# Optimization experiments

Measured on AMD Instinct MI355X. Metric: run time of the kernel, lower is better.

The kernel has to match this reference:

```python
import jax, jax.numpy as jnp
import numpy as np

T, NS, NH, NO = 8192, 512, 1024, 512


def setup_inputs() -> dict:
    key = jax.random.key(0)
    ks = jax.random.split(key, 12)
    f32 = jnp.float32
    x = jax.random.normal(ks[0], (T, NS), f32)
    s = 0.02
    inp = {
        "x": x,
        "w_ih0": jax.random.normal(ks[1], (4 * NH, NS), f32) * s,
        "w_hh0": jax.random.normal(ks[2], (4 * NH, NH), f32) * s,
        "b_ih0": jnp.zeros((4 * NH,), f32),
        "b_hh0": jnp.zeros((4 * NH,), f32),
        "w_ih1": jax.random.normal(ks[3], (4 * NH, NH), f32) * s,
        "w_hh1": jax.random.normal(ks[4], (4 * NH, NH), f32) * s,
        "b_ih1": jnp.zeros((4 * NH,), f32),
        "b_hh1": jnp.zeros((4 * NH,), f32),
        "w_pol": jax.random.normal(ks[5], (NO, NH), f32) * 0.01,
        "b_pol": jax.random.normal(ks[6], (NO,), f32) * 0.01,
        "w_val": jax.random.normal(ks[7], (1, NH), f32) * 0.01,
        "b_val": jax.random.normal(ks[8], (1,), f32) * 0.01,
    }
    return inp


def _lstm_cell(xt, h, c, w_ih, w_hh, b):
    # torch gate order: i, f, g, o
    z = w_ih @ xt + w_hh @ h + b  # [4H]
    i, f, g, o = jnp.split(z, 4)
    i, f, o = jax.nn.sigmoid(i), jax.nn.sigmoid(f), jax.nn.sigmoid(o)
    g = jnp.tanh(g)
    c_new = f * c + i * g
    h_new = o * jnp.tanh(c_new)
    return h_new, c_new


def reference(x, w_ih0, w_hh0, b_ih0, b_hh0, w_ih1, w_hh1, b_ih1, b_hh1,
              w_pol, b_pol, w_val, b_val):
    b0 = b_ih0 + b_hh0
    b1 = b_ih1 + b_hh1
    z = jnp.zeros((NH,), x.dtype)

    def step(carry, xt):
        h0, c0, h1, c1 = carry
        h0, c0 = _lstm_cell(xt, h0, c0, w_ih0, w_hh0, b0)
        h1, c1 = _lstm_cell(h0, h1, c1, w_ih1, w_hh1, b1)
        return (h0, c0, h1, c1), h1

    _, hs = jax.lax.scan(step, (z, z, z, z), x)  # hs: [T, NH]
    policy = jax.nn.softmax(hs @ w_pol.T + b_pol, axis=-1)[:, None, :]  # [T,1,NO]
    values = (hs @ w_val.T + b_val)[:, None, :]  # [T,1,1]
    return policy, values
```

## Files before the change

kernel.cpp:

```cpp
#include <hip/hip_runtime.h>
#include <stdint.h>
#include <stddef.h>

typedef _Float16 f16;
typedef _Float16 half2_t __attribute__((ext_vector_type(2)));
typedef _Float16 half8_t __attribute__((ext_vector_type(8)));
typedef float   float4_t __attribute__((ext_vector_type(4)));
typedef float   float2_t __attribute__((ext_vector_type(2)));

#define T_STEPS 8192
#define L0_BLOCKS 128

#define OFF_ZX   ((size_t)0)
#define OFF_HS   ((size_t)67108864)
#define OFF_R0   (OFF_HS + (size_t)16777216)
#define OFF_R1   (OFF_R0 + (size_t)262144)

__device__ __forceinline__ uint32_t packh(float a, float b) {
  half2_t h; h.x = (_Float16)a; h.y = (_Float16)b;
  return __builtin_bit_cast(uint32_t, h);
}

__device__ __forceinline__ float fdot2w(uint32_t w, uint32_t h, float c) {
#if __has_builtin(__builtin_amdgcn_fdot2)
  return __builtin_amdgcn_fdot2(__builtin_bit_cast(half2_t, w),
                                __builtin_bit_cast(half2_t, h), c, false);
#else
  half2_t a = __builtin_bit_cast(half2_t, w);
  half2_t b = __builtin_bit_cast(half2_t, h);
  return c + (float)a.x * (float)b.x + (float)a.y * (float)b.y;
#endif
}

__device__ __forceinline__ uint64_t ald64(const uint64_t* p) {
  return __hip_atomic_load(p, __ATOMIC_RELAXED, __HIP_MEMORY_SCOPE_AGENT);
}
__device__ __forceinline__ void ast64(uint64_t* p, uint64_t v) {
  __hip_atomic_store(p, v, __ATOMIC_RELAXED, __HIP_MEMORY_SCOPE_AGENT);
}

__device__ __forceinline__ float sigf(float x) { return 1.f / (1.f + __expf(-x)); }
__device__ __forceinline__ float tanhf_(float x) { return 2.f * sigf(2.f * x) - 1.f; }

__global__ void k_init(uint64_t* __restrict__ R) {
  int i = blockIdx.x * blockDim.x + threadIdx.x;
  if (i < (16 + 8) * 4 * 512) R[i] = 0ull;
}

template <bool A16, bool OUT16>
__global__ __launch_bounds__(256) void k_gemm(const void* __restrict__ Ap,
                                              const float* __restrict__ B,
                                              const float* __restrict__ bias0,
                                              const float* __restrict__ bias1,
                                              void* __restrict__ Cp,
                                              int N, int K, int lda) {
  __shared__ __align__(16) f16 As[128 * 40];
  __shared__ __align__(16) f16 Bs[128 * 40];
  int bn = blockIdx.x * 128, bm = blockIdx.y * 128;
  int tid = threadIdx.x;
  int w = tid >> 6, l = tid & 63;
  int m0w = (w >> 1) * 64, n0w = (w & 1) * 64;
  int lr = l & 15, q = l >> 4;
  int srow = tid >> 1, skoff = (tid & 1) * 16;

  float4_t acc[4][4];
#pragma unroll
  for (int i = 0; i < 4; ++i)
#pragma unroll
    for (int j = 0; j < 4; ++j) acc[i][j] = (float4_t){0.f, 0.f, 0.f, 0.f};

  for (int kt = 0; kt < K; kt += 32) {
    __syncthreads();
    if (A16) {
      const f16* Ah = (const f16*)Ap + (size_t)(bm + srow) * lda + kt + skoff;
      uint4 u0 = *(const uint4*)Ah;
      uint4 u1 = *(const uint4*)(Ah + 8);
      *(uint4*)&As[srow * 40 + skoff] = u0;
      *(uint4*)&As[srow * 40 + skoff + 8] = u1;
    } else {
      const float* Af = (const float*)Ap + (size_t)(bm + srow) * lda + kt + skoff;
      const float4_t* A4 = (const float4_t*)Af;
      float4_t f0 = A4[0], f1 = A4[1], f2 = A4[2], f3 = A4[3];
      half8_t h0 = {(f16)f0.x, (f16)f0.y, (f16)f0.z, (f16)f0.w,
                    (f16)f1.x, (f16)f1.y, (f16)f1.z, (f16)f1.w};
      half8_t h1 = {(f16)f2.x, (f16)f2.y, (f16)f2.z, (f16)f2.w,
                    (f16)f3.x, (f16)f3.y, (f16)f3.z, (f16)f3.w};
      *(half8_t*)&As[srow * 40 + skoff] = h0;
      *(half8_t*)&As[srow * 40 + skoff + 8] = h1;
    }
    {
      const float* Bf = B + (size_t)(bn + srow) * K + kt + skoff;
      const float4_t* B4 = (const float4_t*)Bf;
      float4_t f0 = B4[0], f1 = B4[1], f2 = B4[2], f3 = B4[3];
      half8_t h0 = {(f16)f0.x, (f16)f0.y, (f16)f0.z, (f16)f0.w,
                    (f16)f1.x, (f16)f1.y, (f16)f1.z, (f16)f1.w};
      half8_t h1 = {(f16)f2.x, (f16)f2.y, (f16)f2.z, (f16)f2.w,
                    (f16)f3.x, (f16)f3.y, (f16)f3.z, (f16)f3.w};
      *(half8_t*)&Bs[srow * 40 + skoff] = h0;
      *(half8_t*)&Bs[srow * 40 + skoff + 8] = h1;
    }
    __syncthreads();
    half8_t af[4], bf[4];
#pragma unroll
    for (int i = 0; i < 4; ++i) af[i] = *(const half8_t*)&As[(m0w + 16 * i + lr) * 40 + q * 8];
#pragma unroll
    for (int j = 0; j < 4; ++j) bf[j] = *(const half8_t*)&Bs[(n0w + 16 * j + lr) * 40 + q * 8];
#pragma unroll
    for (int i = 0; i < 4; ++i)
#pragma unroll
      for (int j = 0; j < 4; ++j)
        acc[i][j] = __builtin_amdgcn_mfma_f32_16x16x32_f16(af[i], bf[j], acc[i][j], 0, 0, 0);
  }

#pragma unroll
  for (int j = 0; j < 4; ++j) {
    int n = bn + n0w + 16 * j + lr;
    float bv = bias0 ? bias0[n] : 0.f;
    if (bias1) bv += bias1[n];
#pragma unroll
    for (int i = 0; i < 4; ++i) {
#pragma unroll
      for (int r = 0; r < 4; ++r) {
        int m = bm + m0w + 16 * i + q * 4 + r;
        float v = acc[i][j][r] + bv;
        if (OUT16) ((f16*)Cp)[(size_t)m * N + n] = (f16)v;
        else       ((float*)Cp)[(size_t)m * N + n] = v;
      }
    }
  }
}

__global__ __launch_bounds__(256, 1) void k_serial(
    const f16* __restrict__ Zx,
    const float* __restrict__ whh0, const float* __restrict__ wih1,
    const float* __restrict__ whh1,
    uint64_t* __restrict__ R0, uint64_t* __restrict__ R1, f16* __restrict__ hs,
    const float* __restrict__ b_ih1, const float* __restrict__ b_hh1) {
  __shared__ __align__(8) uint32_t hL[1024];
  __shared__ uint32_t pairs[4];

  int tid = threadIdx.x, w = tid >> 6, l = tid & 63;

  if (blockIdx.x < L0_BLOCKS) {
    int b = blockIdx.x;
    uint32_t wr[64];
#pragma unroll
    for (int g = 0; g < 4; ++g)
#pragma unroll
      for (int o = 0; o < 2; ++o) {
        size_t R = (size_t)(1024 * g + 8 * b + 2 * w + o) * 1024;
#pragma unroll
        for (int p = 0; p < 8; ++p) {
          int k = l + 64 * p;
          float2_t u = *(const float2_t*)&whh0[R + 2 * k];
          wr[(2 * g + o) * 8 + p] = packh(u.x, u.y);
        }
      }
    float c0 = 0.f;
    float zx[4] = {0.f, 0.f, 0.f, 0.f};
    if (l < 2) {
#pragma unroll
      for (int g = 0; g < 4; ++g)
        zx[g] = (float)Zx[(size_t)1024 * g + 8 * b + 2 * w + l];
    }

    for (int t = 0; t < T_STEPS; ++t) {
      float zxn[4] = {0.f, 0.f, 0.f, 0.f};
      if (l < 2 && t + 1 < T_STEPS) {
#pragma unroll
        for (int g = 0; g < 4; ++g)
          zxn[g] = (float)Zx[(size_t)(t + 1) * 4096 + 1024 * g + 8 * b + 2 * w + l];
      }
      if (tid == 0 && t >= 2) {
        const uint64_t* lp =
            R1 + ((size_t)(b & 7) * 4 + (size_t)((t - 1) & 3)) * 512 + ((4 * b) & 511);
        while ((int)(uint32_t)(ald64(lp) >> 32) < t - 1) {}
      }
      {
        const uint64_t* base = R0 + ((size_t)(b & 7) * 4 + (size_t)(t & 3)) * 512;
        uint64_t v0 = 0, v1 = 0;
        bool d0 = false, d1 = false;
        do {
          if (!d0) { v0 = ald64(base + tid);       d0 = ((uint32_t)(v0 >> 32) == (uint32_t)t); }
          if (!d1) { v1 = ald64(base + tid + 256); d1 = ((uint32_t)(v1 >> 32) == (uint32_t)t); }
        } while (!(d0 && d1));
        hL[tid] = (uint32_t)v0;
        hL[tid + 256] = (uint32_t)v1;
      }
      __syncthreads();

      uint32_t hw[8];
#pragma unroll
      for (int p = 0; p < 8; ++p) hw[p] = hL[l + 64 * p];
      float acc[8];
#pragma unroll
      for (int ri = 0; ri < 8; ++ri) acc[ri] = 0.f;
#pragma unroll
      for (int ri = 0; ri < 8; ++ri)
#pragma unroll
        for (int p = 0; p < 8; ++p) acc[ri] = fdot2w(wr[ri * 8 + p], hw[p], acc[ri]);
#pragma unroll
      for (int d = 1; d < 64; d <<= 1)
#pragma unroll
        for (int ri = 0; ri < 8; ++ri) acc[ri] += __shfl_xor(acc[ri], d);

      float h = 0.f;
      if (l < 2) {
        float zi = acc[0 + l] + zx[0];
        float zf = acc[2 + l] + zx[1];
        float zg = acc[4 + l] + zx[2];
        float zo = acc[6 + l] + zx[3];
        float ig = sigf(zi), fg = sigf(zf), gg = tanhf_(zg), og = sigf(zo);
        c0 = fg * c0 + ig * gg;
        h = og * tanhf_(c0);
      }
      float ho = __shfl(h, 1);
      if (l == 0) pairs[w] = packh(h, ho);
      __syncthreads();
      if (w == 0) {
        uint64_t val = ((uint64_t)(uint32_t)(t + 1) << 32) | (uint64_t)pairs[l & 3];
        ast64(&R0[((size_t)(l >> 2) * 4 + (size_t)((t + 1) & 3)) * 512 + 4 * b + (l & 3)], val);
      }
#pragma unroll
      for (int g = 0; g < 4; ++g) zx[g] = zxn[g];
    }
  } else {
    int b = blockIdx.x - L0_BLOCKS;
    uint32_t wI[64], wH[64];
#pragma unroll
    for (int g = 0; g < 4; ++g)
#pragma unroll
      for (int o = 0; o < 2; ++o) {
        size_t R = (size_t)(1024 * g + 8 * b + 2 * w + o) * 1024;
#pragma unroll
        for (int p = 0; p < 8; ++p) {
          int k = l + 64 * p;
          float2_t u1 = *(const float2_t*)&wih1[R + 2 * k];
          float2_t u2 = *(const float2_t*)&whh1[R + 2 * k];
          wI[(2 * g + o) * 8 + p] = packh(u1.x, u1.y);
          wH[(2 * g + o) * 8 + p] = packh(u2.x, u2.y);
        }
      }
    float c1 = 0.f;
    float b1v[4] = {0.f, 0.f, 0.f, 0.f};
    if (l < 2) {
#pragma unroll
      for (int g = 0; g < 4; ++g) {
        int r = 1024 * g + 8 * b + 2 * w + l;
        b1v[g] = b_ih1[r] + b_hh1[r];
      }
    }

    for (int t = 0; t < T_STEPS; ++t) {
      {
        const uint64_t* b1p = R1 + ((size_t)(b & 7) * 4 + (size_t)(t & 3)) * 512;
        const uint64_t* b0p = R0 + ((size_t)(8 + (b & 7)) * 4 + (size_t)((t + 1) & 3)) * 512;
        uint64_t v0 = 0, v1 = 0, v2 = 0, v3 = 0;
        bool d0 = false, d1 = false, d2 = false, d3 = false;
        uint32_t tg0 = (uint32_t)(t + 1), tg1 = (uint32_t)t;
        do {
          if (!d0) { v0 = ald64(b0p + tid);       d0 = ((uint32_t)(v0 >> 32) == tg0); }
          if (!d1) { v1 = ald64(b0p + tid + 256); d1 = ((uint32_t)(v1 >> 32) == tg0); }
          if (!d2) { v2 = ald64(b1p + tid);       d2 = ((uint32_t)(v2 >> 32) == tg1); }
          if (!d3) { v3 = ald64(b1p + tid + 256); d3 = ((uint32_t)(v3 >> 32) == tg1); }
        } while (!(d0 && d1 && d2 && d3));
        hL[tid] = (uint32_t)v0;
        hL[tid + 256] = (uint32_t)v1;
        hL[512 + tid] = (uint32_t)v2;
        hL[768 + tid] = (uint32_t)v3;
      }
      __syncthreads();

      uint32_t h0w[8], h1w[8];
#pragma unroll
      for (int p = 0; p < 8; ++p) {
        h0w[p] = hL[l + 64 * p];
        h1w[p] = hL[512 + l + 64 * p];
      }
      float acc[8];
#pragma unroll
      for (int ri = 0; ri < 8; ++ri) acc[ri] = 0.f;
#pragma unroll
      for (int ri = 0; ri < 8; ++ri)
#pragma unroll
        for (int p = 0; p < 8; ++p) {
          acc[ri] = fdot2w(wI[ri * 8 + p], h0w[p], acc[ri]);
          acc[ri] = fdot2w(wH[ri * 8 + p], h1w[p], acc[ri]);
        }
#pragma unroll
      for (int d = 1; d < 64; d <<= 1)
#pragma unroll
        for (int ri = 0; ri < 8; ++ri) acc[ri] += __shfl_xor(acc[ri], d);

      float h = 0.f;
      if (l < 2) {
        float zi = acc[0 + l] + b1v[0];
        float zf = acc[2 + l] + b1v[1];
        float zg = acc[4 + l] + b1v[2];
        float zo = acc[6 + l] + b1v[3];
        float ig = sigf(zi), fg = sigf(zf), gg = tanhf_(zg), og = sigf(zo);
        c1 = fg * c1 + ig * gg;
        h = og * tanhf_(c1);
      }
      float ho = __shfl(h, 1);
      if (l == 0) {
        uint32_t pr = packh(h, ho);
        pairs[w] = pr;
        *(uint32_t*)(hs + (size_t)t * 1024 + 8 * b + 2 * w) = pr;
      }
      __syncthreads();
      if (w == 0 && l < 32) {
        uint64_t val = ((uint64_t)(uint32_t)(t + 1) << 32) | (uint64_t)pairs[l & 3];
        ast64(&R1[((size_t)(l >> 2) * 4 + (size_t)((t + 1) & 3)) * 512 + 4 * b + (l & 3)], val);
      }
    }
  }
}

__global__ void k_values(const f16* __restrict__ hs, const float* __restrict__ w_val,
                         const float* __restrict__ b_val, float* __restrict__ outv) {
  int t = blockIdx.x * 4 + (threadIdx.x >> 6);
  int l = threadIdx.x & 63;
  const f16* row = hs + (size_t)t * 1024 + l * 16;
  const float* wv = w_val + l * 16;
  float s = 0.f;
#pragma unroll
  for (int i = 0; i < 16; ++i) s += (float)row[i] * wv[i];
#pragma unroll
  for (int d = 1; d < 64; d <<= 1) s += __shfl_xor(s, d);
  if (l == 0) outv[t] = s + b_val[0];
}

__global__ void k_softmax(float* __restrict__ out) {
  int t = blockIdx.x * 4 + (threadIdx.x >> 6);
  int l = threadIdx.x & 63;
  float* row = out + (size_t)t * 512;
  float v[8];
  float m = -1e30f;
#pragma unroll
  for (int i = 0; i < 8; ++i) { v[i] = row[l + 64 * i]; m = fmaxf(m, v[i]); }
#pragma unroll
  for (int d = 1; d < 64; d <<= 1) m = fmaxf(m, __shfl_xor(m, d));
  float s = 0.f;
#pragma unroll
  for (int i = 0; i < 8; ++i) { v[i] = __expf(v[i] - m); s += v[i]; }
#pragma unroll
  for (int d = 1; d < 64; d <<= 1) s += __shfl_xor(s, d);
  float inv = 1.f / s;
#pragma unroll
  for (int i = 0; i < 8; ++i) row[l + 64 * i] = v[i] * inv;
}

extern "C" void kernel_launch(void* const* d_in, const int* in_sizes, int n_in,
                              void* d_out, int out_size, void* d_ws, size_t ws_size,
                              hipStream_t stream) {
  const float* x      = (const float*)d_in[0];
  const float* w_ih0  = (const float*)d_in[1];
  const float* w_hh0  = (const float*)d_in[2];
  const float* b_ih0  = (const float*)d_in[3];
  const float* b_hh0  = (const float*)d_in[4];
  const float* w_ih1  = (const float*)d_in[5];
  const float* w_hh1  = (const float*)d_in[6];
  const float* b_ih1  = (const float*)d_in[7];
  const float* b_hh1  = (const float*)d_in[8];
  const float* w_pol  = (const float*)d_in[9];
  const float* b_pol  = (const float*)d_in[10];
  const float* w_val  = (const float*)d_in[11];
  const float* b_val  = (const float*)d_in[12];

  char* ws = (char*)d_ws;
  f16*      Zx  = (f16*)(ws + OFF_ZX);
  f16*      hs  = (f16*)(ws + OFF_HS);
  uint64_t* R0  = (uint64_t*)(ws + OFF_R0);
  uint64_t* R1  = (uint64_t*)(ws + OFF_R1);
  float*    out = (float*)d_out;

  k_init<<<192, 256, 0, stream>>>(R0);
  k_gemm<false, true><<<dim3(32, 64), 256, 0, stream>>>(
      (const void*)x, w_ih0, b_ih0, b_hh0, (void*)Zx, 4096, 512, 512);
  k_serial<<<256, 256, 0, stream>>>(Zx, w_hh0, w_ih1, w_hh1, R0, R1, hs, b_ih1, b_hh1);
  k_gemm<true, false><<<dim3(4, 64), 256, 0, stream>>>(
      (const void*)hs, w_pol, b_pol, nullptr, (void*)out, 512, 1024, 1024);
  k_values<<<2048, 256, 0, stream>>>(hs, w_val, b_val, out + (size_t)8192 * 512);
  k_softmax<<<2048, 256, 0, stream>>>(out);
}
```

Before: 23.47 ms.

## Partition persistent LSTM recurrence by XCD with pipelined layer-1 input projection

Reworks the persistent recurrent kernel into 1024-thread blocks. Each block reads its XCD id and is assigned a role: layer-0 recurrence, layer-1 recurrence, or layer-1 input-projection producers. Layer-0/layer-1 recurrences each run in 32 blocks confined to one XCD and exchange h through XCD-local ring buffers. Layer-1's W_ih·h0 is computed ahead by separate blocks and passed via a tagged ring with progress counters for back-pressure. The intent is to shorten the per-step critical path by keeping tight polling within one XCD's L2 (polling with sc0 loads) and moving work off the serial path. The cost is a complex dependence on the hardware XCD layout, on all blocks being co-resident, and on a role-assignment handshake.

Measured after the change: 34.75 ms. +48.1%, slower.

```diff
diff --git a/kernel.cpp b/kernel.cpp
--- a/kernel.cpp
+++ b/kernel.cpp
@@ -9,18 +9,26 @@
 typedef float   float2_t __attribute__((ext_vector_type(2)));
 
 #define T_STEPS 8192
-#define L0_BLOCKS 128
 
 #define OFF_ZX   ((size_t)0)
 #define OFF_HS   ((size_t)67108864)
-#define OFF_R0   (OFF_HS + (size_t)16777216)
-#define OFF_R1   (OFF_R0 + (size_t)262144)
+#define OFF_R0A  ((size_t)83886080)
+#define OFF_R0B  (OFF_R0A + 131072)
+#define OFF_R1A  (OFF_R0B + 524288)
+#define OFF_ZR   (OFF_R1A + 131072)
+#define OFF_PG0  (OFF_ZR + 1048576)
+#define OFF_PG1  (OFF_PG0 + 8192)
+#define OFF_XC   (OFF_PG1 + 4096)
+#define ZERO_BYTES ((size_t)(OFF_XC + 1024 - OFF_R0A))
 
 __device__ __forceinline__ uint32_t packh(float a, float b) {
   half2_t h; h.x = (_Float16)a; h.y = (_Float16)b;
   return __builtin_bit_cast(uint32_t, h);
 }
-
+__device__ __forceinline__ float hlf(uint32_t u, int i) {
+  half2_t h = __builtin_bit_cast(half2_t, u);
+  return i ? (float)h.y : (float)h.x;
+}
 __device__ __forceinline__ float fdot2w(uint32_t w, uint32_t h, float c) {
 #if __has_builtin(__builtin_amdgcn_fdot2)
   return __builtin_amdgcn_fdot2(__builtin_bit_cast(half2_t, w),
@@ -31,20 +39,60 @@
   return c + (float)a.x * (float)b.x + (float)a.y * (float)b.y;
 #endif
 }
-
 __device__ __forceinline__ uint64_t ald64(const uint64_t* p) {
   return __hip_atomic_load(p, __ATOMIC_RELAXED, __HIP_MEMORY_SCOPE_AGENT);
 }
 __device__ __forceinline__ void ast64(uint64_t* p, uint64_t v) {
   __hip_atomic_store(p, v, __ATOMIC_RELAXED, __HIP_MEMORY_SCOPE_AGENT);
 }
-
+__device__ __forceinline__ uint32_t ald32(const uint32_t* p) {
+  return __hip_atomic_load(p, __ATOMIC_RELAXED, __HIP_MEMORY_SCOPE_AGENT);
+}
+__device__ __forceinline__ void ast32(uint32_t* p, uint32_t v) {
+  __hip_atomic_store(p, v, __ATOMIC_RELAXED, __HIP_MEMORY_SCOPE_AGENT);
+}
+__device__ __forceinline__ uint64_t l2ld64(const uint64_t* p) {
+  uint64_t v;
+  asm volatile("global_load_dwordx2 %0, %1, off sc0\n\ts_waitcnt vmcnt(0)"
+               : "=v"(v) : "v"(p) : "memory");
+  return v;
+}
+__device__ __forceinline__ uint32_t xcc_id() {
+  uint32_t x;
+  asm("s_getreg_b32 %0, hwreg(20, 0, 4)" : "=s"(x));
+  return x;
+}
+__device__ __forceinline__ uint32_t poll_fast(const uint64_t* p, uint32_t tag) {
+  int it = 0;
+  for (;;) {
+    uint64_t v = l2ld64(p);
+    if ((uint32_t)(v >> 32) == tag) return (uint32_t)v;
+    if ((++it & 7) == 7) {
+      v = ald64(p);
+      if ((uint32_t)(v >> 32) == tag) return (uint32_t)v;
+    }
+  }
+}
+__device__ __forceinline__ uint32_t poll_slow(const uint64_t* p, uint32_t tag) {
+  int it = 0;
+  for (;;) {
+    uint64_t v = l2ld64(p);
+    if ((uint32_t)(v >> 32) == tag) return (uint32_t)v;
+    if ((++it & 7) == 7) {
+      v = ald64(p);
+      if ((uint32_t)(v >> 32) == tag) return (uint32_t)v;
+      __builtin_amdgcn_s_sleep(1);
+    }
+  }
+}
 __device__ __forceinline__ float sigf(float x) { return 1.f / (1.f + __expf(-x)); }
 __device__ __forceinline__ float tanhf_(float x) { return 2.f * sigf(2.f * x) - 1.f; }
 
-__global__ void k_init(uint64_t* __restrict__ R) {
-  int i = blockIdx.x * blockDim.x + threadIdx.x;
-  if (i < (16 + 8) * 4 * 512) R[i] = 0ull;
+__global__ void k_init(uint64_t* __restrict__ Z) {
+  size_t n = ZERO_BYTES / 8;
+  for (size_t i = blockIdx.x * blockDim.x + threadIdx.x; i < n;
+       i += (size_t)gridDim.x * blockDim.x)
+    Z[i] = 0ull;
 }
 
 template <bool A16, bool OUT16>
@@ -111,7 +159,6 @@
       for (int j = 0; j < 4; ++j)
         acc[i][j] = __builtin_amdgcn_mfma_f32_16x16x32_f16(af[i], bf[j], acc[i][j], 0, 0, 0);
   }
-
 #pragma unroll
   for (int j = 0; j < 4; ++j) {
     int n = bn + n0w + 16 * j + lr;
@@ -130,191 +177,258 @@
   }
 }
 
-__global__ __launch_bounds__(256, 1) void k_serial(
-    const f16* __restrict__ Zx,
-    const float* __restrict__ whh0, const float* __restrict__ wih1,
-    const float* __restrict__ whh1,
-    uint64_t* __restrict__ R0, uint64_t* __restrict__ R1, f16* __restrict__ hs,
-    const float* __restrict__ b_ih1, const float* __restrict__ b_hh1) {
-  __shared__ __align__(8) uint32_t hL[1024];
-  __shared__ uint32_t pairs[4];
-
+__device__ __forceinline__ void run_l0(int r, const f16* Zx, const float* whh0,
+                                       uint64_t* R0A, uint64_t* R0B,
+                                       const uint32_t* prog0) {
+  __shared__ uint32_t hL[512];
+  __shared__ float zL[4][32];
+  __shared__ uint32_t pairsL[16];
   int tid = threadIdx.x, w = tid >> 6, l = tid & 63;
-
-  if (blockIdx.x < L0_BLOCKS) {
-    int b = blockIdx.x;
-    uint32_t wr[64];
-#pragma unroll
-    for (int g = 0; g < 4; ++g)
-#pragma unroll
-      for (int o = 0; o < 2; ++o) {
-        size_t R = (size_t)(1024 * g + 8 * b + 2 * w + o) * 1024;
-#pragma unroll
-        for (int p = 0; p < 8; ++p) {
-          int k = l + 64 * p;
-          float2_t u = *(const float2_t*)&whh0[R + 2 * k];
-          wr[(2 * g + o) * 8 + p] = packh(u.x, u.y);
-        }
+  int g = w & 3, hh = w >> 2;
+  int O = 32 * r;
+  uint32_t wr[64];
+#pragma unroll
+  for (int j = 0; j < 8; ++j) {
+    size_t R = (size_t)(1024 * g + O + 8 * hh + j) * 1024;
+#pragma unroll
+    for (int p = 0; p < 8; ++p) {
+      int k = l + 64 * p;
+      float2_t u = *(const float2_t*)&whh0[R + 2 * k];
+      wr[j * 8 + p] = packh(u.x, u.y);
+    }
+  }
+  float c0 = 0.f;
+  bool gl = (w == 0 && l < 32);
+  float zx[4] = {0, 0, 0, 0};
+  if (gl)
+#pragma unroll
+    for (int gi = 0; gi < 4; ++gi) zx[gi] = (float)Zx[(size_t)1024 * gi + O + l];
+  uint32_t pw0 = 0, pw1 = 0;
+  const uint32_t* pp0 = prog0 + (2 * r) * 32;
+  const uint32_t* pp1 = prog0 + (2 * r + 1) * 32;
+
+  for (int t = 0; t < T_STEPS; ++t) {
+    float zn[4] = {0, 0, 0, 0};
+    if (gl && t + 1 < T_STEPS)
+#pragma unroll
+      for (int gi = 0; gi < 4; ++gi)
+        zn[gi] = (float)Zx[(size_t)(t + 1) * 4096 + 1024 * gi + O + l];
+    if (tid == 512) {
+      uint32_t pm = pw0 < pw1 ? pw0 : pw1;
+      while (pm + 12 < (uint32_t)t) {
+        pw0 = ald32(pp0); pw1 = ald32(pp1);
+        pm = pw0 < pw1 ? pw0 : pw1;
       }
-    float c0 = 0.f;
-    float zx[4] = {0.f, 0.f, 0.f, 0.f};
-    if (l < 2) {
-#pragma unroll
-      for (int g = 0; g < 4; ++g)
-        zx[g] = (float)Zx[(size_t)1024 * g + 8 * b + 2 * w + l];
-    }
-
-    for (int t = 0; t < T_STEPS; ++t) {
-      float zxn[4] = {0.f, 0.f, 0.f, 0.f};
-      if (l < 2 && t + 1 < T_STEPS) {
-#pragma unroll
-        for (int g = 0; g < 4; ++g)
-          zxn[g] = (float)Zx[(size_t)(t + 1) * 4096 + 1024 * g + 8 * b + 2 * w + l];
-      }
-      if (tid == 0 && t >= 2) {
-        const uint64_t* lp =
-            R1 + ((size_t)(b & 7) * 4 + (size_t)((t - 1) & 3)) * 512 + ((4 * b) & 511);
-        while ((int)(uint32_t)(ald64(lp) >> 32) < t - 1) {}
-      }
-      {
-        const uint64_t* base = R0 + ((size_t)(b & 7) * 4 + (size_t)(t & 3)) * 512;
-        uint64_t v0 = 0, v1 = 0;
-        bool d0 = false, d1 = false;
-        do {
-          if (!d0) { v0 = ald64(base + tid);       d0 = ((uint32_t)(v0 >> 32) == (uint32_t)t); }
-          if (!d1) { v1 = ald64(base + tid + 256); d1 = ((uint32_t)(v1 >> 32) == (uint32_t)t); }
-        } while (!(d0 && d1));
-        hL[tid] = (uint32_t)v0;
-        hL[tid + 256] = (uint32_t)v1;
-      }
-      __syncthreads();
-
-      uint32_t hw[8];
-#pragma unroll
-      for (int p = 0; p < 8; ++p) hw[p] = hL[l + 64 * p];
-      float acc[8];
-#pragma unroll
-      for (int ri = 0; ri < 8; ++ri) acc[ri] = 0.f;
-#pragma unroll
-      for (int ri = 0; ri < 8; ++ri)
-#pragma unroll
-        for (int p = 0; p < 8; ++p) acc[ri] = fdot2w(wr[ri * 8 + p], hw[p], acc[ri]);
-#pragma unroll
-      for (int d = 1; d < 64; d <<= 1)
-#pragma unroll
-        for (int ri = 0; ri < 8; ++ri) acc[ri] += __shfl_xor(acc[ri], d);
-
+    }
+    if (tid < 512)
+      hL[tid] = poll_fast(R0A + ((size_t)((r & 3) * 8 + (t & 7)) * 512 + tid),
+                          (uint32_t)t);
+    __syncthreads();
+    uint32_t hw[8];
+#pragma unroll
+    for (int p = 0; p < 8; ++p) hw[p] = hL[l + 64 * p];
+    float acc[8];
+#pragma unroll
+    for (int j = 0; j < 8; ++j) acc[j] = 0.f;
+#pragma unroll
+    for (int j = 0; j < 8; ++j)
+#pragma unroll
+      for (int p = 0; p < 8; ++p) acc[j] = fdot2w(wr[j * 8 + p], hw[p], acc[j]);
+#pragma unroll
+    for (int d = 1; d < 64; d <<= 1)
+#pragma unroll
+      for (int j = 0; j < 8; ++j) acc[j] += __shfl_xor(acc[j], d);
+    if (l < 8) zL[g][8 * hh + l] = acc[l];
+    __syncthreads();
+    uint32_t tg = (uint32_t)(t + 1);
+    if (w == 0) {
       float h = 0.f;
-      if (l < 2) {
-        float zi = acc[0 + l] + zx[0];
-        float zf = acc[2 + l] + zx[1];
-        float zg = acc[4 + l] + zx[2];
-        float zo = acc[6 + l] + zx[3];
-        float ig = sigf(zi), fg = sigf(zf), gg = tanhf_(zg), og = sigf(zo);
+      if (l < 32) {
+        float zi = zL[0][l] + zx[0], zf = zL[1][l] + zx[1];
+        float zg_ = zL[2][l] + zx[2], zo = zL[3][l] + zx[3];
+        float ig = sigf(zi), fg = sigf(zf), gg = tanhf_(zg_), og = sigf(zo);
         c0 = fg * c0 + ig * gg;
         h = og * tanhf_(c0);
       }
-      float ho = __shfl(h, 1);
-      if (l == 0) pairs[w] = packh(h, ho);
-      __syncthreads();
-      if (w == 0) {
-        uint64_t val = ((uint64_t)(uint32_t)(t + 1) << 32) | (uint64_t)pairs[l & 3];
-        ast64(&R0[((size_t)(l >> 2) * 4 + (size_t)((t + 1) & 3)) * 512 + 4 * b + (l & 3)], val);
-      }
-#pragma unroll
-      for (int g = 0; g < 4; ++g) zx[g] = zxn[g];
-    }
-  } else {
-    int b = blockIdx.x - L0_BLOCKS;
-    uint32_t wI[64], wH[64];
-#pragma unroll
-    for (int g = 0; g < 4; ++g)
-#pragma unroll
-      for (int o = 0; o < 2; ++o) {
-        size_t R = (size_t)(1024 * g + 8 * b + 2 * w + o) * 1024;
-#pragma unroll
-        for (int p = 0; p < 8; ++p) {
-          int k = l + 64 * p;
-          float2_t u1 = *(const float2_t*)&wih1[R + 2 * k];
-          float2_t u2 = *(const float2_t*)&whh1[R + 2 * k];
-          wI[(2 * g + o) * 8 + p] = packh(u1.x, u1.y);
-          wH[(2 * g + o) * 8 + p] = packh(u2.x, u2.y);
-        }
-      }
-    float c1 = 0.f;
-    float b1v[4] = {0.f, 0.f, 0.f, 0.f};
-    if (l < 2) {
-#pragma unroll
-      for (int g = 0; g < 4; ++g) {
-        int r = 1024 * g + 8 * b + 2 * w + l;
-        b1v[g] = b_ih1[r] + b_hh1[r];
-      }
-    }
-
-    for (int t = 0; t < T_STEPS; ++t) {
-      {
-        const uint64_t* b1p = R1 + ((size_t)(b & 7) * 4 + (size_t)(t & 3)) * 512;
-        const uint64_t* b0p = R0 + ((size_t)(8 + (b & 7)) * 4 + (size_t)((t + 1) & 3)) * 512;
-        uint64_t v0 = 0, v1 = 0, v2 = 0, v3 = 0;
-        bool d0 = false, d1 = false, d2 = false, d3 = false;
-        uint32_t tg0 = (uint32_t)(t + 1), tg1 = (uint32_t)t;
-        do {
-          if (!d0) { v0 = ald64(b0p + tid);       d0 = ((uint32_t)(v0 >> 32) == tg0); }
-          if (!d1) { v1 = ald64(b0p + tid + 256); d1 = ((uint32_t)(v1 >> 32) == tg0); }
-          if (!d2) { v2 = ald64(b1p + tid);       d2 = ((uint32_t)(v2 >> 32) == tg1); }
-          if (!d3) { v3 = ald64(b1p + tid + 256); d3 = ((uint32_t)(v3 >> 32) == tg1); }
-        } while (!(d0 && d1 && d2 && d3));
-        hL[tid] = (uint32_t)v0;
-        hL[tid + 256] = (uint32_t)v1;
-        hL[512 + tid] = (uint32_t)v2;
-        hL[768 + tid] = (uint32_t)v3;
-      }
-      __syncthreads();
-
-      uint32_t h0w[8], h1w[8];
-#pragma unroll
-      for (int p = 0; p < 8; ++p) {
-        h0w[p] = hL[l + 64 * p];
-        h1w[p] = hL[512 + l + 64 * p];
-      }
-      float acc[8];
-#pragma unroll
-      for (int ri = 0; ri < 8; ++ri) acc[ri] = 0.f;
-#pragma unroll
-      for (int ri = 0; ri < 8; ++ri)
-#pragma unroll
-        for (int p = 0; p < 8; ++p) {
-          acc[ri] = fdot2w(wI[ri * 8 + p], h0w[p], acc[ri]);
-          acc[ri] = fdot2w(wH[ri * 8 + p], h1w[p], acc[ri]);
-        }
-#pragma unroll
-      for (int d = 1; d < 64; d <<= 1)
-#pragma unroll
-        for (int ri = 0; ri < 8; ++ri) acc[ri] += __shfl_xor(acc[ri], d);
-
+      float hn = __shfl_down(h, 1);
+      uint32_t pr = packh(h, hn);
+      if (l < 32 && !(l & 1)) pairsL[l >> 1] = pr;
+      uint32_t pj = __shfl(pr, 2 * (l & 15));
+      uint64_t val = ((uint64_t)tg << 32) | pj;
+      ast64(R0A + ((size_t)((l >> 4) * 8 + (tg & 7)) * 512 + 16 * r + (l & 15)), val);
+    }
+    __syncthreads();
+    if (tid >= 64 && tid < 192) {
+      int s = tid - 64;
+      uint64_t val = ((uint64_t)tg << 32) | pairsL[s & 15];
+      ast64(R0B + ((size_t)((s >> 4) * 16 + (tg & 15)) * 512 + 16 * r + (s & 15)), val);
+    }
+#pragma unroll
+    for (int gi = 0; gi < 4; ++gi) zx[gi] = zn[gi];
+  }
+}
+
+__device__ __forceinline__ void run_l1(int q, const float* whh1, uint64_t* R1A,
+                                       const uint64_t* ZR, f16* hs,
+                                       uint32_t* prog1) {
+  __shared__ uint32_t hL[512];
+  __shared__ float zL[4][32];
+  __shared__ uint32_t zxL[64];
+  int tid = threadIdx.x, w = tid >> 6, l = tid & 63;
+  int g = w & 3, hh = w >> 2;
+  int O = 32 * q;
+  uint32_t wr[64];
+#pragma unroll
+  for (int j = 0; j < 8; ++j) {
+    size_t R = (size_t)(1024 * g + O + 8 * hh + j) * 1024;
+#pragma unroll
+    for (int p = 0; p < 8; ++p) {
+      int k = l + 64 * p;
+      float2_t u = *(const float2_t*)&whh1[R + 2 * k];
+      wr[j * 8 + p] = packh(u.x, u.y);
+    }
+  }
+  float c1 = 0.f;
+
+  for (int t = 0; t < T_STEPS; ++t) {
+    if (tid < 512) {
+      hL[tid] = poll_fast(R1A + ((size_t)((q & 3) * 8 + (t & 7)) * 512 + tid),
+                          (uint32_t)t);
+    } else if (tid >= 960) {
+      int ii = tid - 960;
+      int gg2 = ii >> 4, i = ii & 15;
+      zxL[ii] = poll_slow(
+          ZR + ((size_t)((q & 3) * 16 + ((t + 1) & 15)) * 2048 + 512 * gg2 + 16 * q + i),
+          (uint32_t)(t + 1));
+    }
+    __syncthreads();
+    if (tid == 512) ast32(prog1 + q * 32, (uint32_t)(t + 1));
+    uint32_t hw[8];
+#pragma unroll
+    for (int p = 0; p < 8; ++p) hw[p] = hL[l + 64 * p];
+    float acc[8];
+#pragma unroll
+    for (int j = 0; j < 8; ++j) acc[j] = 0.f;
+#pragma unroll
+    for (int j = 0; j < 8; ++j)
+#pragma unroll
+      for (int p = 0; p < 8; ++p) acc[j] = fdot2w(wr[j * 8 + p], hw[p], acc[j]);
+#pragma unroll
+    for (int d = 1; d < 64; d <<= 1)
+#pragma unroll
+      for (int j = 0; j < 8; ++j) acc[j] += __shfl_xor(acc[j], d);
+    if (l < 8) zL[g][8 * hh + l] = acc[l];
+    __syncthreads();
+    uint32_t tg = (uint32_t)(t + 1);
+    if (w == 0) {
       float h = 0.f;
-      if (l < 2) {
-        float zi = acc[0 + l] + b1v[0];
-        float zf = acc[2 + l] + b1v[1];
-        float zg = acc[4 + l] + b1v[2];
-        float zo = acc[6 + l] + b1v[3];
-        float ig = sigf(zi), fg = sigf(zf), gg = tanhf_(zg), og = sigf(zo);
+      if (l < 32) {
+        int i2 = l >> 1, hl2 = l & 1;
+        float zi = zL[0][l] + hlf(zxL[i2], hl2);
+        float zf = zL[1][l] + hlf(zxL[16 + i2], hl2);
+        float zg_ = zL[2][l] + hlf(zxL[32 + i2], hl2);
+        float zo = zL[3][l] + hlf(zxL[48 + i2], hl2);
+        float ig = sigf(zi), fg = sigf(zf), gg = tanhf_(zg_), og = sigf(zo);
         c1 = fg * c1 + ig * gg;
         h = og * tanhf_(c1);
       }
-      float ho = __shfl(h, 1);
-      if (l == 0) {
-        uint32_t pr = packh(h, ho);
-        pairs[w] = pr;
-        *(uint32_t*)(hs + (size_t)t * 1024 + 8 * b + 2 * w) = pr;
-      }
-      __syncthreads();
-      if (w == 0 && l < 32) {
-        uint64_t val = ((uint64_t)(uint32_t)(t + 1) << 32) | (uint64_t)pairs[l & 3];
-        ast64(&R1[((size_t)(l >> 2) * 4 + (size_t)((t + 1) & 3)) * 512 + 4 * b + (l & 3)], val);
-      }
-    }
-  }
+      float hn = __shfl_down(h, 1);
+      uint32_t pr = packh(h, hn);
+      if (l < 32 && !(l & 1))
+        ((uint32_t*)hs)[(size_t)t * 512 + 16 * q + (l >> 1)] = pr;
+      uint32_t pj = __shfl(pr, 2 * (l & 15));
+      uint64_t val = ((uint64_t)tg << 32) | pj;
+      ast64(R1A + ((size_t)((l >> 4) * 8 + (tg & 7)) * 512 + 16 * q + (l & 15)), val);
+    }
+  }
+}
+
+__device__ __forceinline__ void run_g1x(int u, const float* wih1,
+                                        const float* b_ih1, const float* b_hh1,
+                                        const uint64_t* R0B, uint64_t* ZR,
+                                        uint32_t* prog0, const uint32_t* prog1) {
+  __shared__ uint32_t hL[512];
+  __shared__ uint32_t zpairs[64];
+  int tid = threadIdx.x, w = tid >> 6, l = tid & 63;
+  int slice = u >> 1, c = u & 1;
+  int RB = 128 * slice;
+  uint32_t wr[64];
+  float bb[8];
+#pragma unroll
+  for (int j = 0; j < 8; ++j) {
+    int row = RB + 8 * w + j;
+    bb[j] = b_ih1[row] + b_hh1[row];
+    size_t R = (size_t)row * 1024;
+#pragma unroll
+    for (int p = 0; p < 8; ++p) {
+      int k = l + 64 * p;
+      float2_t uu = *(const float2_t*)&wih1[R + 2 * k];
+      wr[j * 8 + p] = packh(uu.x, uu.y);
+    }
+  }
+  uint32_t pz = 0;
+  const uint32_t* pp = prog1 + (u & 31) * 32;
+  for (int t = c; t < T_STEPS; t += 2) {
+    if (tid == 520) {
+      while (pz + 8 < (uint32_t)t) pz = ald32(pp);
+    }
+    if (tid < 512)
+      hL[tid] = poll_slow(
+          R0B + ((size_t)((u & 7) * 16 + ((t + 1) & 15)) * 512 + tid),
+          (uint32_t)(t + 1));
+    __syncthreads();
+    if (tid == 512) ast32(prog0 + u * 32, (uint32_t)(t + 1));
+    uint32_t hw[8];
+#pragma unroll
+    for (int p = 0; p < 8; ++p) hw[p] = hL[l + 64 * p];
+    float acc[8];
+#pragma unroll
+    for (int j = 0; j < 8; ++j) acc[j] = 0.f;
+#pragma unroll
+    for (int j = 0; j < 8; ++j)
+#pragma unroll
+      for (int p = 0; p < 8; ++p) acc[j] = fdot2w(wr[j * 8 + p], hw[p], acc[j]);
+#pragma unroll
+    for (int d = 1; d < 64; d <<= 1)
+#pragma unroll
+      for (int j = 0; j < 8; ++j) acc[j] += __shfl_xor(acc[j], d);
+    if (l < 4)
+      zpairs[4 * w + l] = packh(acc[2 * l] + bb[2 * l], acc[2 * l + 1] + bb[2 * l + 1]);
+    __syncthreads();
+    if (tid < 256) {
+      uint64_t val = ((uint64_t)(uint32_t)(t + 1) << 32) | zpairs[tid & 63];
+      ast64(ZR + ((size_t)((tid >> 6) * 16 + ((t + 1) & 15)) * 2048 + 64 * slice + (tid & 63)),
+            val);
+    }
+  }
+}
+
+__global__ __launch_bounds__(1024, 4) void k_serial(
+    const f16* __restrict__ Zx, const float* __restrict__ whh0,
+    const float* __restrict__ wih1, const float* __restrict__ whh1,
+    const float* __restrict__ b_ih1, const float* __restrict__ b_hh1,
+    f16* __restrict__ hs, uint64_t* __restrict__ R0A, uint64_t* __restrict__ R0B,
+    uint64_t* __restrict__ R1A, uint64_t* __restrict__ ZR,
+    uint32_t* __restrict__ prog0, uint32_t* __restrict__ prog1,
+    uint32_t* __restrict__ xc) {
+  __shared__ int srole[2];
+  if (threadIdx.x == 0) {
+    uint32_t xcd = xcc_id() & 7u;
+    uint32_t rk = atomicAdd(&xc[xcd * 16], 1u);
+    atomicOr(&xc[128], 1u << xcd);
+    atomicAdd(&xc[129], 1u);
+    while (ald32(&xc[129]) < (uint32_t)gridDim.x) __builtin_amdgcn_s_sleep(8);
+    uint32_t mask = ald32(&xc[128]);
+    srole[0] = __popc(mask & ((1u << xcd) - 1u));
+    srole[1] = (int)rk;
+  }
+  __syncthreads();
+  int dense = srole[0], rk = srole[1];
+  if (rk >= 32) return;
+  if (dense == 0)      run_l0(rk, Zx, whh0, R0A, R0B, prog0);
+  else if (dense == 1) run_l1(rk, whh1, R1A, ZR, hs, prog1);
+  else if (dense == 2 || dense == 3)
+    run_g1x((dense - 2) * 32 + rk, wih1, b_ih1, b_hh1, R0B, ZR, prog0, prog1);
 }
 
 __global__ void k_values(const f16* __restrict__ hs, const float* __restrict__ w_val,
@@ -369,16 +483,22 @@
   const float* b_val  = (const float*)d_in[12];
 
   char* ws = (char*)d_ws;
-  f16*      Zx  = (f16*)(ws + OFF_ZX);
-  f16*      hs  = (f16*)(ws + OFF_HS);
-  uint64_t* R0  = (uint64_t*)(ws + OFF_R0);
-  uint64_t* R1  = (uint64_t*)(ws + OFF_R1);
-  float*    out = (float*)d_out;
-
-  k_init<<<192, 256, 0, stream>>>(R0);
+  f16*      Zx   = (f16*)(ws + OFF_ZX);
+  f16*      hs   = (f16*)(ws + OFF_HS);
+  uint64_t* R0A  = (uint64_t*)(ws + OFF_R0A);
+  uint64_t* R0B  = (uint64_t*)(ws + OFF_R0B);
+  uint64_t* R1A  = (uint64_t*)(ws + OFF_R1A);
+  uint64_t* ZR   = (uint64_t*)(ws + OFF_ZR);
+  uint32_t* PG0  = (uint32_t*)(ws + OFF_PG0);
+  uint32_t* PG1  = (uint32_t*)(ws + OFF_PG1);
+  uint32_t* XC   = (uint32_t*)(ws + OFF_XC);
+  float*    out  = (float*)d_out;
+
+  k_init<<<256, 256, 0, stream>>>((uint64_t*)(ws + OFF_R0A));
   k_gemm<false, true><<<dim3(32, 64), 256, 0, stream>>>(
       (const void*)x, w_ih0, b_ih0, b_hh0, (void*)Zx, 4096, 512, 512);
-  k_serial<<<256, 256, 0, stream>>>(Zx, w_hh0, w_ih1, w_hh1, R0, R1, hs, b_ih1, b_hh1);
+  k_serial<<<256, 1024, 0, stream>>>(Zx, w_hh0, w_ih1, w_hh1, b_ih1, b_hh1, hs,
+                                     R0A, R0B, R1A, ZR, PG0, PG1, XC);
   k_gemm<true, false><<<dim3(4, 64), 256, 0, stream>>>(
       (const void*)hs, w_pol, b_pol, nullptr, (void*)out, 512, 1024, 1024);
   k_values<<<2048, 256, 0, stream>>>(hs, w_val, b_val, out + (size_t)8192 * 512);
```
